# Performance work log

Hardware: AMD Instinct MI355X
Metric: run time of the kernel (lower is better)

## Reference

```python
import jax, jax.numpy as jnp
import numpy as np

B = 1048576   # batch of independent environments
N = 6         # Izhikevich neurons
STEPS = 10    # neuron update loop iterations per call
NCH = 3       # two-compartment column channels
NPER = 4     # neurons per channel
SUB = 8       # column substeps
# Izhikevich 'RS' parameters
IZ_A, IZ_B, IZ_C, IZ_D = 0.02, 0.2, -65.0, 8.0
I_TONIC = -1.0
DT = 1.0
DT_SUB = 1.0 / SUB
COUPLE = 0.5  # dendrite->soma coupling in the column


def setup_inputs() -> dict:
    key = jax.random.key(0)
    ks = jax.random.split(key, 8)
    f32 = jnp.float32
    return {
        'predator_distance': jax.random.uniform(ks[0], (B,), f32, 0.0, 400.0),
        'closest_conspecific': jax.random.uniform(ks[1], (B,), f32, 0.0, 300.0),
        'ambient_noise': jax.random.uniform(ks[2], (B,), f32),
        'sudden_onset': jax.random.uniform(ks[3], (B,), f32),
        'prev_low': jax.random.uniform(ks[4], (B,), f32),
        'prev_mid': jax.random.uniform(ks[5], (B,), f32),
        'prev_high': jax.random.uniform(ks[6], (B,), f32),
        'v0': jnp.full((B, N), -65.0, f32),
        'u0': jnp.full((B, N), -13.0, f32),   # u = b*v at rest
        'rate0': jnp.zeros((B, N), f32),
        'noise': jax.random.normal(ks[7], (STEPS, B, N), f32),
    }


def _forward(predator_distance, closest_conspecific, ambient_noise, sudden_onset,
             prev_low, prev_mid, prev_high, v0, u0, rate0, noise):
    # --- frequency-band drives (same branchy math as torch, via where) ---
    low = jnp.where(predator_distance < 200.0,
                    jnp.maximum(0.0, (200.0 - predator_distance) / 200.0) ** 2, 0.0)
    mid = jnp.where(closest_conspecific < 150.0,
                    jnp.maximum(0.0, (150.0 - closest_conspecific) / 150.0) * 0.8, 0.0)
    high = jnp.minimum(1.0, ambient_noise * 0.3 + sudden_onset)

    d_low = jnp.abs(low - prev_low)
    d_mid = jnp.abs(mid - prev_mid)
    d_high = jnp.abs(high - prev_high)
    salience = d_low * 0.4 + d_mid * 0.3 + d_high * 0.3

    # startle (refractory counter starts at 0, so only the trigger branch applies)
    startle = (sudden_onset > 0.6) | ((d_low > 0.4) & (low > 0.5))

    # --- input currents [B, 6] ---
    I = jnp.stack([low * 12.0, low * 8.0, mid * 12.0, mid * 8.0,
                   high * 12.0, high * 8.0], axis=-1)

    # --- 10-step Izhikevich loop as a scan over pre-generated noise ---
    def iz_step(carry, nz):
        v, u, rate = carry
        Iin = I + nz * 0.3 + I_TONIC
        v = v + DT * (0.04 * v * v + 5.0 * v + 140.0 - u + Iin)
        u = u + DT * IZ_A * (IZ_B * v - u)
        spike = v >= 30.0
        v = jnp.where(spike, IZ_C, v)
        u = jnp.where(spike, u + IZ_D, u)
        rate = 0.9 * rate + 0.1 * spike.astype(v.dtype)
        return (v, u, rate), None

    (v, u, rate), _ = jax.lax.scan(iz_step, (v0, u0, rate0), noise)

    # --- two-compartment predictive-coding column (3 channels, 4 per ch, 8 substeps)
    # NOTE: torch code updates _prev_* BEFORE building the prediction tensor,
    # so prediction_drive == sensory_drive (faithful reproduction).
    sensory = jnp.stack([low, mid, high], axis=-1)      # [B, 3]
    prediction = sensory                                 # [B, 3]

    vd0 = jnp.zeros((NCH, NPER), sensory.dtype)
    vs0 = jnp.zeros((NCH, NPER), sensory.dtype)
    vd0 = jnp.broadcast_to(vd0, sensory.shape[:1] + (NCH, NPER))
    vs0 = jnp.broadcast_to(vs0, sensory.shape[:1] + (NCH, NPER))

    def col_step(carry, _):
        vd, vs = carry
        vd = vd + DT_SUB * (-vd + prediction[..., None])
        vs = vs + DT_SUB * (-vs + sensory[..., None] + COUPLE * vd)
        return (vd, vs), None

    (vd, vs), _ = jax.lax.scan(col_step, (vd0, vs0), None, length=SUB)

    pe = vs.mean(-1) - vd.mean(-1)                       # [B, 3]
    precision = 1.0 / (1.0 + pe * pe)                    # [B, 3]
    # F = sum_ch 0.5*pi*pe^2 - 0.5*log(pi)
    free_energy = jnp.sum(0.5 * precision * pe * pe + 0.5 * jnp.log1p(pe * pe), axis=-1)

    pe_mean = jnp.abs(pe).mean(-1)
    prec_mean = precision.mean(-1)
    rate_mean = rate.mean(-1)

    out = jnp.stack([low, mid, high, salience, pe_mean, prec_mean,
                     free_energy, rate_mean], axis=-1)   # [B, 8]
    return out, startle


def reference(predator_distance, closest_conspecific, ambient_noise, sudden_onset,
              prev_low, prev_mid, prev_high, v0, u0, rate0, noise):
    return _forward(predator_distance, closest_conspecific, ambient_noise, sudden_onset,
                    prev_low, prev_mid, prev_high, v0, u0, rate0, noise)
```

## Files before the change

kernel.cpp:

```cpp
#include <hip/hip_runtime.h>


#define STEPS 10
#define NNEUR 6

__global__ __launch_bounds__(256) void spiking_auditory_kernel(
    const float* __restrict__ pd_in, const float* __restrict__ cc_in,
    const float* __restrict__ an_in, const float* __restrict__ so_in,
    const float* __restrict__ pl_in, const float* __restrict__ pm_in,
    const float* __restrict__ ph_in,
    const float* __restrict__ v0_in, const float* __restrict__ u0_in,
    const float* __restrict__ r0_in, const float* __restrict__ noise_in,
    float* __restrict__ out, int B)
{
#pragma clang fp contract(off)
    int b = blockIdx.x * blockDim.x + threadIdx.x;
    if (b >= B) return;

    float pd = pd_in[b], cc = cc_in[b], an = an_in[b], so = so_in[b];
    float pl = pl_in[b], pm = pm_in[b], ph = ph_in[b];

    float low = 0.0f;
    if (pd < 200.0f) {
        float t = (200.0f - pd) / 200.0f;
        t = fmaxf(0.0f, t);
        low = t * t;
    }
    float mid = 0.0f;
    if (cc < 150.0f) {
        float t = (150.0f - cc) / 150.0f;
        t = fmaxf(0.0f, t);
        mid = t * 0.8f;
    }
    float high = fminf(1.0f, (an * 0.3f) + so);

    float d_low  = fabsf(low - pl);
    float d_mid  = fabsf(mid - pm);
    float d_high = fabsf(high - ph);
    float salience = ((d_low * 0.4f) + (d_mid * 0.3f)) + (d_high * 0.3f);

    bool startle = (so > 0.6f) || ((d_low > 0.4f) && (low > 0.5f));

    float I[NNEUR];
    I[0] = low * 12.0f;  I[1] = low * 8.0f;
    I[2] = mid * 12.0f;  I[3] = mid * 8.0f;
    I[4] = high * 12.0f; I[5] = high * 8.0f;

    size_t base6 = (size_t)b * NNEUR;
    float v[NNEUR], u[NNEUR], rate[NNEUR];
    {
        float2 a = *(const float2*)(v0_in + base6);
        float2 c = *(const float2*)(v0_in + base6 + 2);
        float2 e = *(const float2*)(v0_in + base6 + 4);
        v[0]=a.x; v[1]=a.y; v[2]=c.x; v[3]=c.y; v[4]=e.x; v[5]=e.y;
    }
    {
        float2 a = *(const float2*)(u0_in + base6);
        float2 c = *(const float2*)(u0_in + base6 + 2);
        float2 e = *(const float2*)(u0_in + base6 + 4);
        u[0]=a.x; u[1]=a.y; u[2]=c.x; u[3]=c.y; u[4]=e.x; u[5]=e.y;
    }
    {
        float2 a = *(const float2*)(r0_in + base6);
        float2 c = *(const float2*)(r0_in + base6 + 2);
        float2 e = *(const float2*)(r0_in + base6 + 4);
        rate[0]=a.x; rate[1]=a.y; rate[2]=c.x; rate[3]=c.y; rate[4]=e.x; rate[5]=e.y;
    }

    size_t step_stride = (size_t)B * NNEUR;
    const float* nz_base = noise_in + base6;
    #pragma unroll
    for (int s = 0; s < STEPS; ++s) {
        const float* nzp = nz_base + (size_t)s * step_stride;
        float2 n0 = *(const float2*)(nzp);
        float2 n1 = *(const float2*)(nzp + 2);
        float2 n2 = *(const float2*)(nzp + 4);
        float nz[NNEUR] = {n0.x, n0.y, n1.x, n1.y, n2.x, n2.y};
        #pragma unroll
        for (int n = 0; n < NNEUR; ++n) {
            float Iin = (I[n] + (nz[n] * 0.3f)) + (-1.0f);
            float vv = v[n];
            float t = ((0.04f * vv) * vv) + (5.0f * vv);
            t = t + 140.0f;
            t = t - u[n];
            t = t + Iin;
            vv = vv + t;
            float uu = u[n] + (0.02f * ((0.2f * vv) - u[n]));
            bool spike = (vv >= 30.0f);
            v[n] = spike ? -65.0f : vv;
            u[n] = spike ? (uu + 8.0f) : uu;
            rate[n] = (0.9f * rate[n]) + (0.1f * (spike ? 1.0f : 0.0f));
        }
    }

    float sens[3] = {low, mid, high};
    float fe = 0.0f, pe_abs_sum = 0.0f, prec_sum = 0.0f;
    #pragma unroll
    for (int ch = 0; ch < 3; ++ch) {
        float sv = sens[ch];
        float vd = 0.0f, vs = 0.0f;
        #pragma unroll
        for (int t = 0; t < 8; ++t) {
            vd = vd + (0.125f * ((-vd) + sv));
            vs = vs + (0.125f * (((-vs) + sv) + (0.5f * vd)));
        }
        float pe  = vs - vd;
        float pe2 = pe * pe;
        float pr  = 1.0f / (1.0f + pe2);
        fe = fe + ((0.5f * pr) * pe2 + 0.5f * log1pf(pe2));
        pe_abs_sum = pe_abs_sum + fabsf(pe);
        prec_sum   = prec_sum + pr;
    }
    float pe_mean   = pe_abs_sum / 3.0f;
    float prec_mean = prec_sum / 3.0f;

    float rsum = ((((rate[0] + rate[1]) + rate[2]) + rate[3]) + rate[4]) + rate[5];
    float rate_mean = rsum / 6.0f;

    float4 o0 = make_float4(low, mid, high, salience);
    float4 o1 = make_float4(pe_mean, prec_mean, fe, rate_mean);
    *(float4*)(out + (size_t)b * 8)     = o0;
    *(float4*)(out + (size_t)b * 8 + 4) = o1;
    out[(size_t)B * 8 + b] = startle ? 1.0f : 0.0f;
}

extern "C" void kernel_launch(void* const* d_in, const int* in_sizes, int n_in,
                              void* d_out, int out_size, void* d_ws, size_t ws_size,
                              hipStream_t stream) {
    const float* pd = (const float*)d_in[0];
    const float* cc = (const float*)d_in[1];
    const float* an = (const float*)d_in[2];
    const float* so = (const float*)d_in[3];
    const float* pl = (const float*)d_in[4];
    const float* pm = (const float*)d_in[5];
    const float* ph = (const float*)d_in[6];
    const float* v0 = (const float*)d_in[7];
    const float* u0 = (const float*)d_in[8];
    const float* r0 = (const float*)d_in[9];
    const float* nz = (const float*)d_in[10];
    float* out = (float*)d_out;
    int B = in_sizes[0];

    int block = 256;
    int grid = (B + block - 1) / block;
    spiking_auditory_kernel<<<grid, block, 0, stream>>>(
        pd, cc, an, so, pl, pm, ph, v0, u0, r0, nz, out, B);
}
```

Measured before the change: 426.6 us.

## Split each environment across three threads, one per neuron pair

Each environment is now handled by three threads, each simulating one band's two neurons. Loads of v/u/rate/noise become contiguous float2 per thread, so each wave accesses memory fully coalesced, and all ten noise steps are prefetched up front. Rate sums are combined through LDS with a block barrier. In exchange, the per-env scalar inputs and the column computation are redundantly repeated three times, and the out-of-range tail relies on clamped loads that could read past the buffers when B is not a multiple of 256.

```diff
diff --git a/kernel.cpp b/kernel.cpp
--- a/kernel.cpp
+++ b/kernel.cpp
@@ -2,9 +2,10 @@
 
 
 #define STEPS 10
-#define NNEUR 6
+#define ENVS_PER_BLOCK 256
+#define BLOCK (ENVS_PER_BLOCK * 3)
 
-__global__ __launch_bounds__(256) void spiking_auditory_kernel(
+__global__ __launch_bounds__(BLOCK) void spiking_auditory_kernel(
     const float* __restrict__ pd_in, const float* __restrict__ cc_in,
     const float* __restrict__ an_in, const float* __restrict__ so_in,
     const float* __restrict__ pl_in, const float* __restrict__ pm_in,
@@ -14,23 +15,28 @@
     float* __restrict__ out, int B)
 {
 #pragma clang fp contract(off)
-    int b = blockIdx.x * blockDim.x + threadIdx.x;
-    if (b >= B) return;
+    __shared__ float lds_rate[BLOCK * 2];
 
-    float pd = pd_in[b], cc = cc_in[b], an = an_in[b], so = so_in[b];
-    float pl = pl_in[b], pm = pm_in[b], ph = ph_in[b];
+    int t = threadIdx.x;
+    int env_local = t / 3;
+    int c = t - env_local * 3;
+    int env = blockIdx.x * ENVS_PER_BLOCK + env_local;
+    int env_ld = min(env, B - 1);
+
+    float pd = pd_in[env_ld], cc = cc_in[env_ld], an = an_in[env_ld], so = so_in[env_ld];
+    float pl = pl_in[env_ld], pm = pm_in[env_ld], ph = ph_in[env_ld];
 
     float low = 0.0f;
     if (pd < 200.0f) {
-        float t = (200.0f - pd) / 200.0f;
-        t = fmaxf(0.0f, t);
-        low = t * t;
+        float x = (200.0f - pd) / 200.0f;
+        x = fmaxf(0.0f, x);
+        low = x * x;
     }
     float mid = 0.0f;
     if (cc < 150.0f) {
-        float t = (150.0f - cc) / 150.0f;
-        t = fmaxf(0.0f, t);
-        mid = t * 0.8f;
+        float x = (150.0f - cc) / 150.0f;
+        x = fmaxf(0.0f, x);
+        mid = x * 0.8f;
     }
     float high = fminf(1.0f, (an * 0.3f) + so);
 
@@ -38,69 +44,69 @@
     float d_mid  = fabsf(mid - pm);
     float d_high = fabsf(high - ph);
     float salience = ((d_low * 0.4f) + (d_mid * 0.3f)) + (d_high * 0.3f);
-
     bool startle = (so > 0.6f) || ((d_low > 0.4f) && (low > 0.5f));
 
-    float I[NNEUR];
-    I[0] = low * 12.0f;  I[1] = low * 8.0f;
-    I[2] = mid * 12.0f;  I[3] = mid * 8.0f;
-    I[4] = high * 12.0f; I[5] = high * 8.0f;
+    float band = (c == 0) ? low : ((c == 1) ? mid : high);
+    float Ia = band * 12.0f;
+    float Ib = band * 8.0f;
 
-    size_t base6 = (size_t)b * NNEUR;
-    float v[NNEUR], u[NNEUR], rate[NNEUR];
-    {
-        float2 a = *(const float2*)(v0_in + base6);
-        float2 c = *(const float2*)(v0_in + base6 + 2);
-        float2 e = *(const float2*)(v0_in + base6 + 4);
-        v[0]=a.x; v[1]=a.y; v[2]=c.x; v[3]=c.y; v[4]=e.x; v[5]=e.y;
-    }
-    {
-        float2 a = *(const float2*)(u0_in + base6);
-        float2 c = *(const float2*)(u0_in + base6 + 2);
-        float2 e = *(const float2*)(u0_in + base6 + 4);
-        u[0]=a.x; u[1]=a.y; u[2]=c.x; u[3]=c.y; u[4]=e.x; u[5]=e.y;
-    }
-    {
-        float2 a = *(const float2*)(r0_in + base6);
-        float2 c = *(const float2*)(r0_in + base6 + 2);
-        float2 e = *(const float2*)(r0_in + base6 + 4);
-        rate[0]=a.x; rate[1]=a.y; rate[2]=c.x; rate[3]=c.y; rate[4]=e.x; rate[5]=e.y;
-    }
+    size_t base = (size_t)blockIdx.x * (ENVS_PER_BLOCK * 6) + 2 * (size_t)t;
+    float2 v2 = *(const float2*)(v0_in + base);
+    float2 u2 = *(const float2*)(u0_in + base);
+    float2 r2 = *(const float2*)(r0_in + base);
+    float va = v2.x, vb = v2.y, ua = u2.x, ub = u2.y, ra = r2.x, rb = r2.y;
 
-    size_t step_stride = (size_t)B * NNEUR;
-    const float* nz_base = noise_in + base6;
+    size_t step6 = (size_t)B * 6;
+    const float* npz = noise_in + base;
+    float2 nzv[STEPS];
+    #pragma unroll
+    for (int s = 0; s < STEPS; ++s)
+        nzv[s] = *(const float2*)(npz + (size_t)s * step6);
+
     #pragma unroll
     for (int s = 0; s < STEPS; ++s) {
-        const float* nzp = nz_base + (size_t)s * step_stride;
-        float2 n0 = *(const float2*)(nzp);
-        float2 n1 = *(const float2*)(nzp + 2);
-        float2 n2 = *(const float2*)(nzp + 4);
-        float nz[NNEUR] = {n0.x, n0.y, n1.x, n1.y, n2.x, n2.y};
-        #pragma unroll
-        for (int n = 0; n < NNEUR; ++n) {
-            float Iin = (I[n] + (nz[n] * 0.3f)) + (-1.0f);
-            float vv = v[n];
-            float t = ((0.04f * vv) * vv) + (5.0f * vv);
-            t = t + 140.0f;
-            t = t - u[n];
-            t = t + Iin;
-            vv = vv + t;
-            float uu = u[n] + (0.02f * ((0.2f * vv) - u[n]));
+        {
+            float Iin = (Ia + (nzv[s].x * 0.3f)) + (-1.0f);
+            float vv = va;
+            float x = ((0.04f * vv) * vv) + (5.0f * vv);
+            x = x + 140.0f;  x = x - ua;  x = x + Iin;
+            vv = vv + x;
+            float uu = ua + (0.02f * ((0.2f * vv) - ua));
             bool spike = (vv >= 30.0f);
-            v[n] = spike ? -65.0f : vv;
-            u[n] = spike ? (uu + 8.0f) : uu;
-            rate[n] = (0.9f * rate[n]) + (0.1f * (spike ? 1.0f : 0.0f));
+            va = spike ? -65.0f : vv;
+            ua = spike ? (uu + 8.0f) : uu;
+            ra = (0.9f * ra) + (0.1f * (spike ? 1.0f : 0.0f));
+        }
+        {
+            float Iin = (Ib + (nzv[s].y * 0.3f)) + (-1.0f);
+            float vv = vb;
+            float x = ((0.04f * vv) * vv) + (5.0f * vv);
+            x = x + 140.0f;  x = x - ub;  x = x + Iin;
+            vv = vv + x;
+            float uu = ub + (0.02f * ((0.2f * vv) - ub));
+            bool spike = (vv >= 30.0f);
+            vb = spike ? -65.0f : vv;
+            ub = spike ? (uu + 8.0f) : uu;
+            rb = (0.9f * rb) + (0.1f * (spike ? 1.0f : 0.0f));
         }
     }
 
-    float sens[3] = {low, mid, high};
+    lds_rate[2 * t]     = ra;
+    lds_rate[2 * t + 1] = rb;
+    __syncthreads();
+    const float* rp = lds_rate + 6 * env_local;
+    float rsum = ((((rp[0] + rp[1]) + rp[2]) + rp[3]) + rp[4]) + rp[5];
+    float rate_mean = rsum / 6.0f;
+
+    float sens0 = low, sens1 = mid, sens2 = high;
     float fe = 0.0f, pe_abs_sum = 0.0f, prec_sum = 0.0f;
+    float sarr[3] = {sens0, sens1, sens2};
     #pragma unroll
     for (int ch = 0; ch < 3; ++ch) {
-        float sv = sens[ch];
+        float sv = sarr[ch];
         float vd = 0.0f, vs = 0.0f;
         #pragma unroll
-        for (int t = 0; t < 8; ++t) {
+        for (int k = 0; k < 8; ++k) {
             vd = vd + (0.125f * ((-vd) + sv));
             vs = vs + (0.125f * (((-vs) + sv) + (0.5f * vd)));
         }
@@ -114,14 +120,16 @@
     float pe_mean   = pe_abs_sum / 3.0f;
     float prec_mean = prec_sum / 3.0f;
 
-    float rsum = ((((rate[0] + rate[1]) + rate[2]) + rate[3]) + rate[4]) + rate[5];
-    float rate_mean = rsum / 6.0f;
-
-    float4 o0 = make_float4(low, mid, high, salience);
-    float4 o1 = make_float4(pe_mean, prec_mean, fe, rate_mean);
-    *(float4*)(out + (size_t)b * 8)     = o0;
-    *(float4*)(out + (size_t)b * 8 + 4) = o1;
-    out[(size_t)B * 8 + b] = startle ? 1.0f : 0.0f;
+    if (env < B) {
+        if (c == 0) {
+            *(float4*)(out + (size_t)env * 8) = make_float4(low, mid, high, salience);
+        } else if (c == 1) {
+            *(float4*)(out + (size_t)env * 8 + 4) =
+                make_float4(pe_mean, prec_mean, fe, rate_mean);
+        } else {
+            out[(size_t)B * 8 + env] = startle ? 1.0f : 0.0f;
+        }
+    }
 }
 
 extern "C" void kernel_launch(void* const* d_in, const int* in_sizes, int n_in,
@@ -141,8 +149,7 @@
     float* out = (float*)d_out;
     int B = in_sizes[0];
 
-    int block = 256;
-    int grid = (B + block - 1) / block;
-    spiking_auditory_kernel<<<grid, block, 0, stream>>>(
+    int grid = (B + ENVS_PER_BLOCK - 1) / ENVS_PER_BLOCK;
+    spiking_auditory_kernel<<<grid, BLOCK, 0, stream>>>(
         pd, cc, an, so, pl, pm, ph, v0, u0, r0, nz, out, B);
 }
```

New measurement: 426.7 us. About the same (+0.0%).
